# Performance work log

Hardware: AMD Instinct MI355X
Metric: run time of the kernel (lower is better)

Reference implementation:

```python
import jax, jax.numpy as jnp
import numpy as np
from jax.ops import segment_sum

N_NODES = 50000
N_EDGES = 800000
IN_DIM, H1, H2, OUT_DIM = 256, 640, 320, 128


def _glorot(key, fan_in, fan_out):
    lim = np.sqrt(6.0 / (fan_in + fan_out)).astype(np.float32)
    return jax.random.uniform(key, (fan_in, fan_out), jnp.float32, -lim, lim)


def setup_inputs() -> dict:
    key = jax.random.key(0)
    ks = jax.random.split(key, 12)
    features = jax.random.normal(ks[0], (N_NODES, IN_DIM), jnp.float32)
    edge_src = jax.random.randint(ks[1], (N_EDGES,), 0, N_NODES)
    edge_dst = jax.random.randint(ks[2], (N_EDGES,), 0, N_NODES)
    return {
        "features": features,
        "edge_src": edge_src,
        "edge_dst": edge_dst,
        "W1_self": _glorot(ks[3], IN_DIM, H1),
        "W1_neigh": _glorot(ks[4], IN_DIM, H1),
        "b1": jnp.zeros((H1,), jnp.float32),
        "W2_self": _glorot(ks[5], H1, H2),
        "W2_neigh": _glorot(ks[6], H1, H2),
        "b2": jnp.zeros((H2,), jnp.float32),
        "W3_self": _glorot(ks[7], H2, OUT_DIM),
        "W3_neigh": _glorot(ks[8], H2, OUT_DIM),
        "b3": jnp.zeros((OUT_DIM,), jnp.float32),
        "Wres": _glorot(ks[9], IN_DIM, OUT_DIM),
        "bres": jnp.zeros((OUT_DIM,), jnp.float32),
    }


def _sage_mean(h, edge_src, edge_dst, inv_deg, W_self, W_neigh, b):
    # mean-aggregate over in-neighbors: gather source feats, segment-sum by dst
    agg = segment_sum(h[edge_src], edge_dst, num_segments=N_NODES)  # [N, d]
    h_neigh = agg * inv_deg[:, None]
    return h @ W_self + h_neigh @ W_neigh + b


def reference(features, edge_src, edge_dst,
              W1_self, W1_neigh, b1,
              W2_self, W2_neigh, b2,
              W3_self, W3_neigh, b3,
              Wres, bres):
    deg = segment_sum(jnp.ones((N_EDGES,), jnp.float32), edge_dst,
                      num_segments=N_NODES)
    inv_deg = jnp.where(deg > 0, 1.0 / jnp.maximum(deg, 1.0), 0.0)

    res = jax.nn.elu(features @ Wres + bres)
    # dropout(p=0.2) is identity at inference
    x = jax.nn.elu(_sage_mean(features, edge_src, edge_dst, inv_deg,
                              W1_self, W1_neigh, b1))
    x = jax.nn.elu(_sage_mean(x, edge_src, edge_dst, inv_deg,
                              W2_self, W2_neigh, b2))
    x = jax.nn.elu(_sage_mean(x, edge_src, edge_dst, inv_deg,
                              W3_self, W3_neigh, b3))
    return (x, res)
```

## Files before the change

kernel.cpp:

```cpp
#include <hip/hip_runtime.h>
#include <hip/hip_bf16.h>
#include <cstdint>
#include <cstddef>

#define N_NODES 50000
#define N_EDGES 800000
#define IN_DIM 256
#define H1 640
#define H2 320
#define OUT_DIM 128

typedef unsigned short u16;
typedef __attribute__((ext_vector_type(8))) short short8v;
typedef __attribute__((ext_vector_type(4))) float float4v;

__device__ __forceinline__ float b2f(u16 u) {
    union { unsigned int i; float f; } v; v.i = ((unsigned int)u) << 16; return v.f;
}
__device__ __forceinline__ u16 f2b(float f) {
    __hip_bfloat16 h = __float2bfloat16(f);
    return *reinterpret_cast<u16*>(&h);
}


#define SCAN_BLK 256
#define SCAN_NB  ((N_NODES + SCAN_BLK - 1) / SCAN_BLK)

__global__ void zero2_kernel(int* __restrict__ a, int* __restrict__ b, int n) {
    int i = blockIdx.x * blockDim.x + threadIdx.x;
    if (i < n) { a[i] = 0; b[i] = 0; }
}

__global__ void count_deg_kernel(const int* __restrict__ dst, int* __restrict__ cnt, int nE) {
    int i = blockIdx.x * blockDim.x + threadIdx.x;
    if (i < nE) atomicAdd(&cnt[dst[i]], 1);
}

__global__ __launch_bounds__(SCAN_BLK)
void block_sum_kernel(const int* __restrict__ cnt, int* __restrict__ bsum) {
    __shared__ int red[SCAN_BLK];
    int t = threadIdx.x;
    int i = blockIdx.x * SCAN_BLK + t;
    red[t] = (i < N_NODES) ? cnt[i] : 0;
    __syncthreads();
#pragma unroll
    for (int off = SCAN_BLK / 2; off > 0; off >>= 1) {
        if (t < off) red[t] += red[t + off];
        __syncthreads();
    }
    if (t == 0) bsum[blockIdx.x] = red[0];
}

__global__ __launch_bounds__(SCAN_BLK)
void scan_bsum_kernel(const int* __restrict__ bsum, int* __restrict__ boff) {
    __shared__ int s[SCAN_BLK];
    int t = threadIdx.x;
    s[t] = (t < SCAN_NB) ? bsum[t] : 0;
    __syncthreads();
#pragma unroll
    for (int off = 1; off < SCAN_BLK; off <<= 1) {
        int v = (t >= off) ? s[t - off] : 0;
        __syncthreads();
        s[t] += v;
        __syncthreads();
    }
    if (t < SCAN_NB) boff[t] = (t == 0) ? 0 : s[t - 1];
}

__global__ __launch_bounds__(SCAN_BLK)
void final_scan_kernel(const int* __restrict__ cnt, const int* __restrict__ boff,
                       int* __restrict__ row_ptr, float* __restrict__ inv_deg) {
    __shared__ int s[SCAN_BLK];
    int b = blockIdx.x, t = threadIdx.x;
    int i = b * SCAN_BLK + t;
    int v = (i < N_NODES) ? cnt[i] : 0;
    s[t] = v;
    __syncthreads();
#pragma unroll
    for (int off = 1; off < SCAN_BLK; off <<= 1) {
        int u = (t >= off) ? s[t - off] : 0;
        __syncthreads();
        s[t] += u;
        __syncthreads();
    }
    if (i < N_NODES) {
        int base = boff[b];
        int incl = s[t];
        row_ptr[i] = base + incl - v;
        inv_deg[i] = (v > 0) ? (1.0f / (float)v) : 0.0f;
        if (i == N_NODES - 1) row_ptr[N_NODES] = base + incl;
    }
}

__global__ void scatter_kernel(const int* __restrict__ src, const int* __restrict__ dst,
                               const int* __restrict__ row_ptr, int* __restrict__ cursor,
                               int* __restrict__ csr_src, int nE) {
    int i = blockIdx.x * blockDim.x + threadIdx.x;
    if (i < nE) {
        int d = dst[i];
        int p = atomicAdd(&cursor[d], 1);
        csr_src[row_ptr[d] + p] = src[i];
    }
}


__global__ void cast_kernel(const float4* __restrict__ in, ushort4* __restrict__ out, int n4) {
    int i = blockIdx.x * blockDim.x + threadIdx.x;
    if (i < n4) {
        float4 v = in[i];
        ushort4 o;
        o.x = f2b(v.x); o.y = f2b(v.y); o.z = f2b(v.z); o.w = f2b(v.w);
        out[i] = o;
    }
}


__global__ __launch_bounds__(256)
void transpose_cast_kernel(const float* __restrict__ in, u16* __restrict__ out,
                           int K, int N) {
    __shared__ float t[32][33];
    int bx = blockIdx.x * 32;
    int by = blockIdx.y * 32;
    int x = threadIdx.x;
    int y = threadIdx.y;
#pragma unroll
    for (int i = 0; i < 32; i += 8) {
        int r = by + y + i, c = bx + x;
        if (r < K && c < N) t[y + i][x] = in[(size_t)r * N + c];
    }
    __syncthreads();
#pragma unroll
    for (int i = 0; i < 32; i += 8) {
        int r = bx + y + i, c = by + x;
        if (r < N && c < K) out[(size_t)r * K + c] = f2b(t[x][y + i]);
    }
}


#define AGG_GRID 2048

template<int D, int MODE>
__global__ __launch_bounds__(256, 8)
void aggregate_kernel(const u16* __restrict__ h, const int* __restrict__ row_ptr,
                      const int* __restrict__ csr_src, const float* __restrict__ inv_deg,
                      const void* __restrict__ T, const float* __restrict__ bias,
                      void* __restrict__ out) {
    constexpr int L = D / 8;
    constexpr int NPW = (64 / L) >= 1 ? (64 / L) : 1;
    int tid = threadIdx.x;
    int wave = tid >> 6, lane = tid & 63;
    int sub = lane / L, cl = lane % L;
    if (sub >= NPW) return;

    float bv[8];
    if (MODE != 0) {
        const float* bp = bias + cl * 8;
        float4 ba = *(const float4*)bp, bb = *(const float4*)(bp + 4);
        bv[0] = ba.x; bv[1] = ba.y; bv[2] = ba.z; bv[3] = ba.w;
        bv[4] = bb.x; bv[5] = bb.y; bv[6] = bb.z; bv[7] = bb.w;
    }

    const u16* __restrict__ hb = h + cl * 8;
    const int stride = gridDim.x * 4 * NPW;
    for (int node = (blockIdx.x * 4 + wave) * NPW + sub; node < N_NODES; node += stride) {
        int e0 = row_ptr[node], e1 = row_ptr[node + 1];
        float acc[8];
#pragma unroll
        for (int j = 0; j < 8; ++j) acc[j] = 0.0f;

        for (int e = e0; e < e1; e += 4) {
            int idx[4]; float msk[4];
#pragma unroll
            for (int u = 0; u < 4; ++u) {
                int ee = e + u;
                msk[u] = (ee < e1) ? 1.0f : 0.0f;
                idx[u] = csr_src[(ee < e1) ? ee : e];
            }
            short8v v[4];
#pragma unroll
            for (int u = 0; u < 4; ++u)
                v[u] = *(const short8v*)(hb + (size_t)idx[u] * D);
#pragma unroll
            for (int u = 0; u < 4; ++u)
#pragma unroll
                for (int j = 0; j < 8; ++j)
                    acc[j] += msk[u] * b2f((u16)v[u][j]);
        }

        float w = inv_deg[node];
        if (MODE == 0) {
            short8v o;
#pragma unroll
            for (int j = 0; j < 8; ++j) o[j] = (short)f2b(acc[j] * w);
            *(short8v*)((u16*)out + (size_t)node * D + cl * 8) = o;
        } else if (MODE == 1) {
            short8v tb = *(const short8v*)((const u16*)T + (size_t)node * D + cl * 8);
            short8v o;
#pragma unroll
            for (int j = 0; j < 8; ++j) {
                float x = acc[j] * w + b2f((u16)tb[j]) + bv[j];
                x = (x > 0.0f) ? x : expm1f(x);
                o[j] = (short)f2b(x);
            }
            *(short8v*)((u16*)out + (size_t)node * D + cl * 8) = o;
        } else {
            const float* tp = (const float*)T + (size_t)node * D + cl * 8;
            float4 ta = *(const float4*)tp, tb4 = *(const float4*)(tp + 4);
            float tv[8] = {ta.x, ta.y, ta.z, ta.w, tb4.x, tb4.y, tb4.z, tb4.w};
            float v8[8];
#pragma unroll
            for (int j = 0; j < 8; ++j) {
                float x = acc[j] * w + tv[j] + bv[j];
                v8[j] = (x > 0.0f) ? x : expm1f(x);
            }
            float* op = (float*)out + (size_t)node * D + cl * 8;
            *(float4*)op = make_float4(v8[0], v8[1], v8[2], v8[3]);
            *(float4*)(op + 4) = make_float4(v8[4], v8[5], v8[6], v8[7]);
        }
    }
}


template<bool DUAL, int EPI>
__global__ __launch_bounds__(256)
void mfma_gemm_kernel(const u16* __restrict__ A0, const u16* __restrict__ A1,
                      const u16* __restrict__ W0T, const u16* __restrict__ W1T,
                      const float* __restrict__ bias,
                      void* __restrict__ C0, void* __restrict__ C1,
                      int M, int K, int N, int N0, int gx) {
    int nwg = gridDim.x;
    int d = blockIdx.x;
    int q = nwg >> 3, r8 = nwg & 7;
    int xcd = d & 7, idx = d >> 3;
    int flat = (xcd < r8 ? xcd * (q + 1) : r8 * (q + 1) + (xcd - r8) * q) + idx;
    int bxt = flat % gx, byt = flat / gx;

    int tid = threadIdx.x;
    int wid = tid >> 6;
    int lane = tid & 63;
    int lr = lane & 15;
    int lb = lane >> 4;
    int wr = wid >> 1;
    int wc = wid & 1;

    int bm = byt * 128;
    int bn = bxt * 128;

    __shared__ u16 smem[2 * 8192];

    const int NT0 = K >> 5;
    const int NT = DUAL ? (NT0 * 2) : NT0;

    auto stage = [&](int kt, int buf) {
        const u16* Ap; const u16* Wp; int kk;
        if (DUAL && kt >= NT0) { Ap = A1; Wp = W1T; kk = (kt - NT0) << 5; }
        else                   { Ap = A0; Wp = W0T; kk = kt << 5; }
        u16* ab = smem + buf * 8192;
#pragma unroll
        for (int i = 0; i < 2; ++i) {
            int cc = tid + i * 256;
            int rr = cc >> 2, c = cc & 3;
            int cg = c ^ (rr & 3);
            int grow = bm + rr; if (grow > M - 1) grow = M - 1;
            const u16* gp = Ap + (size_t)grow * K + kk + cg * 8;
            __builtin_amdgcn_global_load_lds(
                (const __attribute__((address_space(1))) void*)gp,
                (__attribute__((address_space(3))) void*)(ab + cc * 8), 16, 0, 0);
        }
#pragma unroll
        for (int i = 0; i < 2; ++i) {
            int cc = tid + i * 256;
            int rr = cc >> 2, c = cc & 3;
            int cg = c ^ (rr & 3);
            int gcol = bn + rr;
            const u16* gp = Wp + (size_t)gcol * K + kk + cg * 8;
            __builtin_amdgcn_global_load_lds(
                (const __attribute__((address_space(1))) void*)gp,
                (__attribute__((address_space(3))) void*)(ab + 4096 + cc * 8), 16, 0, 0);
        }
    };

    float4v acc[4][4] = {};

    int cur = 0;
    stage(0, 0);
    __syncthreads();

    int sw = lb ^ (lr & 3);
    for (int kt = 0; kt < NT; ++kt) {
        if (kt + 1 < NT) stage(kt + 1, cur ^ 1);
        const u16* ab = smem + cur * 8192;
        const u16* bb = ab + 4096;
        short8v af[4], bf[4];
#pragma unroll
        for (int i = 0; i < 4; ++i)
            af[i] = *(const short8v*)(ab + (wr * 64 + i * 16 + lr) * 32 + sw * 8);
#pragma unroll
        for (int j = 0; j < 4; ++j)
            bf[j] = *(const short8v*)(bb + (wc * 64 + j * 16 + lr) * 32 + sw * 8);
#pragma unroll
        for (int i = 0; i < 4; ++i)
#pragma unroll
            for (int j = 0; j < 4; ++j)
                acc[i][j] = __builtin_amdgcn_mfma_f32_16x16x32_bf16(
                    af[i], bf[j], acc[i][j], 0, 0, 0);
        __syncthreads();
        cur ^= 1;
    }

    int bmw = bm + wr * 64, bnw = bn + wc * 64;
    if (EPI <= 1) {
        float bi[4];
#pragma unroll
        for (int j = 0; j < 4; ++j) bi[j] = bias[bnw + j * 16 + lr];
#pragma unroll
        for (int i = 0; i < 4; ++i) {
#pragma unroll
            for (int rr = 0; rr < 4; ++rr) {
                int row = bmw + i * 16 + lb * 4 + rr;
                if (row >= M) continue;
#pragma unroll
                for (int j = 0; j < 4; ++j) {
                    int col = bnw + j * 16 + lr;
                    float v = acc[i][j][rr] + bi[j];
                    v = (v > 0.0f) ? v : expm1f(v);
                    if (EPI == 1) ((float*)C0)[(size_t)row * N + col] = v;
                    else          ((u16*)C0)[(size_t)row * N + col] = f2b(v);
                }
            }
        }
    } else {
        int N1 = N - N0;
#pragma unroll
        for (int i = 0; i < 4; ++i) {
#pragma unroll
            for (int rr = 0; rr < 4; ++rr) {
                int row = bmw + i * 16 + lb * 4 + rr;
                if (row >= M) continue;
#pragma unroll
                for (int j = 0; j < 4; ++j) {
                    int col = bnw + j * 16 + lr;
                    float v = acc[i][j][rr];
                    if (col < N0) {
                        ((u16*)C0)[(size_t)row * N0 + col] = f2b(v);
                    } else {
                        int c1 = col - N0;
                        if (EPI == 3) ((float*)C1)[(size_t)row * N1 + c1] = v;
                        else          ((u16*)C1)[(size_t)row * N1 + c1] = f2b(v);
                    }
                }
            }
        }
    }
}


extern "C" void kernel_launch(void* const* d_in, const int* in_sizes, int n_in,
                              void* d_out, int out_size, void* d_ws, size_t ws_size,
                              hipStream_t stream) {
    const float* features = (const float*)d_in[0];
    const int*   edge_src = (const int*)d_in[1];
    const int*   edge_dst = (const int*)d_in[2];
    const float* W1s = (const float*)d_in[3];
    const float* W1n = (const float*)d_in[4];
    const float* b1  = (const float*)d_in[5];
    const float* W2s = (const float*)d_in[6];
    const float* W2n = (const float*)d_in[7];
    const float* b2  = (const float*)d_in[8];
    const float* W3s = (const float*)d_in[9];
    const float* W3n = (const float*)d_in[10];
    const float* b3  = (const float*)d_in[11];
    const float* Wres = (const float*)d_in[12];
    const float* bres = (const float*)d_in[13];

    float* out_x   = (float*)d_out;
    float* out_res = out_x + (size_t)N_NODES * OUT_DIM;

    size_t off = 0;
    auto carve = [&](size_t bytes) {
        size_t p = off;
        off += (bytes + 255) & ~(size_t)255;
        return p;
    };
    size_t o_cnt     = carve((size_t)N_NODES * 4);
    size_t o_rowptr  = carve((size_t)(N_NODES + 1) * 4);
    size_t o_cursor  = carve((size_t)N_NODES * 4);
    size_t o_invdeg  = carve((size_t)N_NODES * 4);
    size_t o_csr     = carve((size_t)N_EDGES * 4);
    size_t o_bsum    = carve((size_t)SCAN_NB * 4);
    size_t o_boff    = carve((size_t)SCAN_NB * 4);
    size_t o_w1s  = carve((size_t)IN_DIM * H1 * 2);
    size_t o_w1n  = carve((size_t)IN_DIM * H1 * 2);
    size_t o_w23  = carve((size_t)H1 * (H2 + H2) * 2);
    size_t o_w3   = carve((size_t)H2 * (OUT_DIM * 2) * 2);
    size_t o_wrs  = carve((size_t)IN_DIM * OUT_DIM * 2);
    size_t o_regA = carve((size_t)N_NODES * (IN_DIM + IN_DIM) * 2);
    size_t o_regB = carve((size_t)N_NODES * H1 * 2);
    size_t o_regC = carve((size_t)N_NODES * H2 * 2);
    size_t o_regD = carve((size_t)N_NODES * H2 * 2);
    size_t REQUIRED = off;
    if (ws_size < REQUIRED) return;

    char* W = (char*)d_ws;
    int*   cnt     = (int*)(W + o_cnt);
    int*   row_ptr = (int*)(W + o_rowptr);
    int*   cursor  = (int*)(W + o_cursor);
    float* inv_deg = (float*)(W + o_invdeg);
    int*   csr_src = (int*)(W + o_csr);
    int*   bsum    = (int*)(W + o_bsum);
    int*   boff    = (int*)(W + o_boff);
    u16* W1sT = (u16*)(W + o_w1s);
    u16* W1nT = (u16*)(W + o_w1n);
    u16* W23T = (u16*)(W + o_w23);
    u16* W3T  = (u16*)(W + o_w3);
    u16* WrsT = (u16*)(W + o_wrs);
    u16* fX   = (u16*)(W + o_regA);
    u16* aggF = fX + (size_t)N_NODES * IN_DIM;
    u16* x2   = (u16*)(W + o_regA);
    u16* x1   = (u16*)(W + o_regB);
    u16* Y3   = (u16*)(W + o_regB);
    float* T3 = (float*)(W + o_regB + (size_t)N_NODES * OUT_DIM * 2);
    u16* Y2   = (u16*)(W + o_regC);
    u16* T2   = (u16*)(W + o_regD);

    const int mt = (N_NODES + 127) / 128;

    zero2_kernel<<<(N_NODES + 255) / 256, 256, 0, stream>>>(cnt, cursor, N_NODES);
    count_deg_kernel<<<(N_EDGES + 255) / 256, 256, 0, stream>>>(edge_dst, cnt, N_EDGES);
    block_sum_kernel<<<SCAN_NB, SCAN_BLK, 0, stream>>>(cnt, bsum);
    scan_bsum_kernel<<<1, SCAN_BLK, 0, stream>>>(bsum, boff);
    final_scan_kernel<<<SCAN_NB, SCAN_BLK, 0, stream>>>(cnt, boff, row_ptr, inv_deg);
    scatter_kernel<<<(N_EDGES + 255) / 256, 256, 0, stream>>>(edge_src, edge_dst, row_ptr,
                                                              cursor, csr_src, N_EDGES);

    {
        int n4 = N_NODES * IN_DIM / 4;
        cast_kernel<<<(n4 + 255) / 256, 256, 0, stream>>>((const float4*)features,
                                                          (ushort4*)fX, n4);
    }
    {
        dim3 b(32, 8);
        dim3 g1(H1 / 32, IN_DIM / 32);
        transpose_cast_kernel<<<g1, b, 0, stream>>>(W1s, W1sT, IN_DIM, H1);
        transpose_cast_kernel<<<g1, b, 0, stream>>>(W1n, W1nT, IN_DIM, H1);
        dim3 g2(H2 / 32, H1 / 32);
        transpose_cast_kernel<<<g2, b, 0, stream>>>(W2n, W23T, H1, H2);
        transpose_cast_kernel<<<g2, b, 0, stream>>>(W2s, W23T + (size_t)H2 * H1, H1, H2);
        dim3 g3(OUT_DIM / 32, H2 / 32);
        transpose_cast_kernel<<<g3, b, 0, stream>>>(W3n, W3T, H2, OUT_DIM);
        transpose_cast_kernel<<<g3, b, 0, stream>>>(W3s, W3T + (size_t)OUT_DIM * H2, H2, OUT_DIM);
        dim3 g4(OUT_DIM / 32, IN_DIM / 32);
        transpose_cast_kernel<<<g4, b, 0, stream>>>(Wres, WrsT, IN_DIM, OUT_DIM);
    }

    mfma_gemm_kernel<false, 1><<<1 * mt, 256, 0, stream>>>(
        fX, nullptr, WrsT, nullptr, bres, out_res, nullptr,
        N_NODES, IN_DIM, OUT_DIM, OUT_DIM, 1);

    aggregate_kernel<IN_DIM, 0><<<AGG_GRID, 256, 0, stream>>>(
        fX, row_ptr, csr_src, inv_deg, nullptr, nullptr, aggF);
    mfma_gemm_kernel<true, 0><<<(H1 / 128) * mt, 256, 0, stream>>>(
        fX, aggF, W1sT, W1nT, b1, x1, nullptr,
        N_NODES, IN_DIM, H1, H1, H1 / 128);

    mfma_gemm_kernel<false, 2><<<((H2 * 2) / 128) * mt, 256, 0, stream>>>(
        x1, nullptr, W23T, nullptr, nullptr, Y2, T2,
        N_NODES, H1, H2 * 2, H2, (H2 * 2) / 128);
    aggregate_kernel<H2, 1><<<AGG_GRID, 256, 0, stream>>>(
        Y2, row_ptr, csr_src, inv_deg, T2, b2, x2);

    mfma_gemm_kernel<false, 3><<<((OUT_DIM * 2) / 128) * mt, 256, 0, stream>>>(
        x2, nullptr, W3T, nullptr, nullptr, Y3, T3,
        N_NODES, H2, OUT_DIM * 2, OUT_DIM, (OUT_DIM * 2) / 128);
    aggregate_kernel<OUT_DIM, 2><<<AGG_GRID, 256, 0, stream>>>(
        Y3, row_ptr, csr_src, inv_deg, T3, b3, out_x);
}
```

Measured before the change: 464.6 us.

## Fuse residual GEMM into layer-1 dual GEMM and batch weight transposes

Appends the residual weight as extra output columns of the layer-1 dual GEMM, with zero-padded neighbor weights for those columns, so the features are read once and the separate residual GEMM launch goes away. A new epilogue routes the residual tiles to fp32 output with their own bias. The seven weight transposes become a single launch indexed by blockIdx.z. The aggregation kernel's node-to-thread mapping changes from per-wave grouping to per-block grouping, which matters for D=320 where lanes were previously idle. The cost is some wasted MFMA work on the zero neighbor weights for the residual columns.

```diff
diff --git a/kernel.cpp b/kernel.cpp
--- a/kernel.cpp
+++ b/kernel.cpp
@@ -116,11 +116,26 @@
 
 
 __global__ __launch_bounds__(256)
-void transpose_cast_kernel(const float* __restrict__ in, u16* __restrict__ out,
-                           int K, int N) {
-    __shared__ float t[32][33];
+void transpose_all_kernel(const float* __restrict__ W1s, const float* __restrict__ Wres,
+                          const float* __restrict__ W1n, const float* __restrict__ W2n,
+                          const float* __restrict__ W2s, const float* __restrict__ W3n,
+                          const float* __restrict__ W3s,
+                          u16* __restrict__ W1T, u16* __restrict__ W1nT,
+                          u16* __restrict__ W23T, u16* __restrict__ W3T) {
+    const float* in; u16* out; int K, N, rowOff;
+    switch (blockIdx.z) {
+        case 0: in = W1s;  out = W1T;  K = 256; N = 640; rowOff = 0;   break;
+        case 1: in = Wres; out = W1T;  K = 256; N = 128; rowOff = 640; break;
+        case 2: in = W1n;  out = W1nT; K = 256; N = 640; rowOff = 0;   break;
+        case 3: in = W2n;  out = W23T; K = 640; N = 320; rowOff = 0;   break;
+        case 4: in = W2s;  out = W23T; K = 640; N = 320; rowOff = 320; break;
+        case 5: in = W3n;  out = W3T;  K = 320; N = 128; rowOff = 0;   break;
+        default: in = W3s; out = W3T;  K = 320; N = 128; rowOff = 128; break;
+    }
     int bx = blockIdx.x * 32;
     int by = blockIdx.y * 32;
+    if (bx >= N || by >= K) return;
+    __shared__ float t[32][33];
     int x = threadIdx.x;
     int y = threadIdx.y;
 #pragma unroll
@@ -132,7 +147,7 @@
 #pragma unroll
     for (int i = 0; i < 32; i += 8) {
         int r = bx + y + i, c = by + x;
-        if (r < N && c < K) out[(size_t)r * K + c] = f2b(t[x][y + i]);
+        if (r < N && c < K) out[(size_t)(rowOff + r) * K + c] = f2b(t[x][y + i]);
     }
 }
 
@@ -146,11 +161,10 @@
                       const void* __restrict__ T, const float* __restrict__ bias,
                       void* __restrict__ out) {
     constexpr int L = D / 8;
-    constexpr int NPW = (64 / L) >= 1 ? (64 / L) : 1;
-    int tid = threadIdx.x;
-    int wave = tid >> 6, lane = tid & 63;
-    int sub = lane / L, cl = lane % L;
-    if (sub >= NPW) return;
+    constexpr int GPB = 256 / L;
+    int t = threadIdx.x;
+    int g = t / L, cl = t % L;
+    if (g >= GPB) return;
 
     float bv[8];
     if (MODE != 0) {
@@ -161,8 +175,8 @@
     }
 
     const u16* __restrict__ hb = h + cl * 8;
-    const int stride = gridDim.x * 4 * NPW;
-    for (int node = (blockIdx.x * 4 + wave) * NPW + sub; node < N_NODES; node += stride) {
+    const int stride = gridDim.x * GPB;
+    for (int node = blockIdx.x * GPB + g; node < N_NODES; node += stride) {
         int e0 = row_ptr[node], e1 = row_ptr[node + 1];
         float acc[8];
 #pragma unroll
@@ -225,7 +239,7 @@
 __global__ __launch_bounds__(256)
 void mfma_gemm_kernel(const u16* __restrict__ A0, const u16* __restrict__ A1,
                       const u16* __restrict__ W0T, const u16* __restrict__ W1T,
-                      const float* __restrict__ bias,
+                      const float* __restrict__ bias, const float* __restrict__ bias2,
                       void* __restrict__ C0, void* __restrict__ C1,
                       int M, int K, int N, int N0, int gx) {
     int nwg = gridDim.x;
@@ -309,7 +323,7 @@
     }
 
     int bmw = bm + wr * 64, bnw = bn + wc * 64;
-    if (EPI <= 1) {
+    if (EPI == 0) {
         float bi[4];
 #pragma unroll
         for (int j = 0; j < 4; ++j) bi[j] = bias[bnw + j * 16 + lr];
@@ -324,8 +338,32 @@
                     int col = bnw + j * 16 + lr;
                     float v = acc[i][j][rr] + bi[j];
                     v = (v > 0.0f) ? v : expm1f(v);
-                    if (EPI == 1) ((float*)C0)[(size_t)row * N + col] = v;
-                    else          ((u16*)C0)[(size_t)row * N + col] = f2b(v);
+                    ((u16*)C0)[(size_t)row * N + col] = f2b(v);
+                }
+            }
+        }
+    } else if (EPI == 4) {
+        bool resTile = (bnw >= N0);
+        int N1 = N - N0;
+        float bi[4];
+#pragma unroll
+        for (int j = 0; j < 4; ++j) {
+            int c = bnw + j * 16 + lr;
+            bi[j] = resTile ? bias2[c - N0] : bias[c];
+        }
+#pragma unroll
+        for (int i = 0; i < 4; ++i) {
+#pragma unroll
+            for (int rr = 0; rr < 4; ++rr) {
+                int row = bmw + i * 16 + lb * 4 + rr;
+                if (row >= M) continue;
+#pragma unroll
+                for (int j = 0; j < 4; ++j) {
+                    int col = bnw + j * 16 + lr;
+                    float v = acc[i][j][rr] + bi[j];
+                    v = (v > 0.0f) ? v : expm1f(v);
+                    if (resTile) ((float*)C1)[(size_t)row * N1 + (col - N0)] = v;
+                    else         ((u16*)C0)[(size_t)row * N0 + col] = f2b(v);
                 }
             }
         }
@@ -389,11 +427,10 @@
     size_t o_csr     = carve((size_t)N_EDGES * 4);
     size_t o_bsum    = carve((size_t)SCAN_NB * 4);
     size_t o_boff    = carve((size_t)SCAN_NB * 4);
-    size_t o_w1s  = carve((size_t)IN_DIM * H1 * 2);
-    size_t o_w1n  = carve((size_t)IN_DIM * H1 * 2);
+    size_t o_w1   = carve((size_t)(H1 + OUT_DIM) * IN_DIM * 2);
+    size_t o_w1n  = carve((size_t)(H1 + OUT_DIM) * IN_DIM * 2);
     size_t o_w23  = carve((size_t)H1 * (H2 + H2) * 2);
     size_t o_w3   = carve((size_t)H2 * (OUT_DIM * 2) * 2);
-    size_t o_wrs  = carve((size_t)IN_DIM * OUT_DIM * 2);
     size_t o_regA = carve((size_t)N_NODES * (IN_DIM + IN_DIM) * 2);
     size_t o_regB = carve((size_t)N_NODES * H1 * 2);
     size_t o_regC = carve((size_t)N_NODES * H2 * 2);
@@ -409,11 +446,10 @@
     int*   csr_src = (int*)(W + o_csr);
     int*   bsum    = (int*)(W + o_bsum);
     int*   boff    = (int*)(W + o_boff);
-    u16* W1sT = (u16*)(W + o_w1s);
+    u16* W1T  = (u16*)(W + o_w1);
     u16* W1nT = (u16*)(W + o_w1n);
     u16* W23T = (u16*)(W + o_w23);
     u16* W3T  = (u16*)(W + o_w3);
-    u16* WrsT = (u16*)(W + o_wrs);
     u16* fX   = (u16*)(W + o_regA);
     u16* aggF = fX + (size_t)N_NODES * IN_DIM;
     u16* x2   = (u16*)(W + o_regA);
@@ -439,38 +475,27 @@
                                                           (ushort4*)fX, n4);
     }
     {
-        dim3 b(32, 8);
-        dim3 g1(H1 / 32, IN_DIM / 32);
-        transpose_cast_kernel<<<g1, b, 0, stream>>>(W1s, W1sT, IN_DIM, H1);
-        transpose_cast_kernel<<<g1, b, 0, stream>>>(W1n, W1nT, IN_DIM, H1);
-        dim3 g2(H2 / 32, H1 / 32);
-        transpose_cast_kernel<<<g2, b, 0, stream>>>(W2n, W23T, H1, H2);
-        transpose_cast_kernel<<<g2, b, 0, stream>>>(W2s, W23T + (size_t)H2 * H1, H1, H2);
-        dim3 g3(OUT_DIM / 32, H2 / 32);
-        transpose_cast_kernel<<<g3, b, 0, stream>>>(W3n, W3T, H2, OUT_DIM);
-        transpose_cast_kernel<<<g3, b, 0, stream>>>(W3s, W3T + (size_t)OUT_DIM * H2, H2, OUT_DIM);
-        dim3 g4(OUT_DIM / 32, IN_DIM / 32);
-        transpose_cast_kernel<<<g4, b, 0, stream>>>(Wres, WrsT, IN_DIM, OUT_DIM);
-    }
-
-    mfma_gemm_kernel<false, 1><<<1 * mt, 256, 0, stream>>>(
-        fX, nullptr, WrsT, nullptr, bres, out_res, nullptr,
-        N_NODES, IN_DIM, OUT_DIM, OUT_DIM, 1);
+        int* pad = (int*)(W1nT + (size_t)H1 * IN_DIM);
+        zero2_kernel<<<(8192 + 255) / 256, 256, 0, stream>>>(pad, pad, 8192);
+        dim3 b(32, 8), g(20, 20, 7);
+        transpose_all_kernel<<<g, b, 0, stream>>>(W1s, Wres, W1n, W2n, W2s, W3n, W3s,
+                                                  W1T, W1nT, W23T, W3T);
+    }
 
     aggregate_kernel<IN_DIM, 0><<<AGG_GRID, 256, 0, stream>>>(
         fX, row_ptr, csr_src, inv_deg, nullptr, nullptr, aggF);
-    mfma_gemm_kernel<true, 0><<<(H1 / 128) * mt, 256, 0, stream>>>(
-        fX, aggF, W1sT, W1nT, b1, x1, nullptr,
-        N_NODES, IN_DIM, H1, H1, H1 / 128);
+    mfma_gemm_kernel<true, 4><<<((H1 + OUT_DIM) / 128) * mt, 256, 0, stream>>>(
+        fX, aggF, W1T, W1nT, b1, bres, x1, out_res,
+        N_NODES, IN_DIM, H1 + OUT_DIM, H1, (H1 + OUT_DIM) / 128);
 
     mfma_gemm_kernel<false, 2><<<((H2 * 2) / 128) * mt, 256, 0, stream>>>(
-        x1, nullptr, W23T, nullptr, nullptr, Y2, T2,
+        x1, nullptr, W23T, nullptr, nullptr, nullptr, Y2, T2,
         N_NODES, H1, H2 * 2, H2, (H2 * 2) / 128);
     aggregate_kernel<H2, 1><<<AGG_GRID, 256, 0, stream>>>(
         Y2, row_ptr, csr_src, inv_deg, T2, b2, x2);
 
     mfma_gemm_kernel<false, 3><<<((OUT_DIM * 2) / 128) * mt, 256, 0, stream>>>(
-        x2, nullptr, W3T, nullptr, nullptr, Y3, T3,
+        x2, nullptr, W3T, nullptr, nullptr, nullptr, Y3, T3,
         N_NODES, H2, OUT_DIM * 2, OUT_DIM, (OUT_DIM * 2) / 128);
     aggregate_kernel<OUT_DIM, 2><<<AGG_GRID, 256, 0, stream>>>(
         Y3, row_ptr, csr_src, inv_deg, T3, b3, out_x);
```

After: 462.2 us. About the same (-0.5%).
